# Performance work log

Measured on AMD Instinct MI355X. Metric: run time of the kernel, lower is better.

Reference implementation:

```python
import jax, jax.numpy as jnp
import numpy as np

N, IN_F, OUT_F, EMB = 8192, 256, 128, 16

def setup_inputs() -> dict:
    key = jax.random.key(0)
    ks = jax.random.split(key, 6)
    s_in, s_out = 1.0 / np.sqrt(IN_F), 1.0 / np.sqrt(OUT_F)
    return {
        "h": jax.random.normal(ks[0], (N, IN_F), jnp.float32),
        "eps": jax.random.normal(ks[1], (N, OUT_F), jnp.float32),
        "a_str": jax.random.uniform(ks[2], (N, N), jnp.float32),  # precomputed exp_adj kernel (positive)
        "W_fc": jax.random.normal(ks[3], (IN_F, OUT_F), jnp.float32) * s_in,
        "W_k": jax.random.normal(ks[4], (OUT_F, EMB), jnp.float32) * s_out,
        "W_q": jax.random.normal(ks[5], (OUT_F, EMB), jnp.float32) * s_out,
    }

def reference(h, eps, a_str, W_fc, W_k, W_q):
    # h0 = fc(h); h <- N(0,1) sample (eps) + h0
    hh = eps + h @ W_fc                      # [N, OUT_F]
    k = hh @ W_k                             # [N, EMB]
    q = hh @ W_q                             # [N, EMB]
    a_att = jax.nn.softmax(k @ q.T, axis=-1) # [N, N]
    a = a_str * a_att                        # elementwise structural mask
    a = a / jnp.sum(a, axis=-1, keepdims=True)  # renormalize rows
    return a @ hh                            # [N, OUT_F]
```

## Files before the change

### kernel.cpp

```cpp
#include <hip/hip_runtime.h>
#include <hip/hip_bf16.h>

#define NN   8192
#define INF_ 256
#define OF   128
#define EMBD 16
#define QB   32
#define JB   128
#define NST  (NN / JB)

typedef __attribute__((ext_vector_type(4))) float f32x4;
typedef __attribute__((ext_vector_type(8))) short s16x8;

__device__ __forceinline__ unsigned short f2bf(float x) {
  unsigned u = __builtin_bit_cast(unsigned, x);
  return (unsigned short)((u + 0x7FFFu + ((u >> 16) & 1u)) >> 16);
}

__device__ __forceinline__ float fexp2(float x) {
#if __has_builtin(__builtin_amdgcn_exp2f)
  return __builtin_amdgcn_exp2f(x);
#else
  return exp2f(x);
#endif
}

__global__ __launch_bounds__(256) void k_hh(const float* __restrict__ h,
                                            const float* __restrict__ eps,
                                            const float* __restrict__ Wfc,
                                            float* __restrict__ hh) {
  const int o  = threadIdx.x & (OF - 1);
  const int rh = threadIdx.x >> 7;
  const int i0 = blockIdx.x * 8 + rh * 4;
  float a0 = eps[(size_t)(i0 + 0) * OF + o];
  float a1 = eps[(size_t)(i0 + 1) * OF + o];
  float a2 = eps[(size_t)(i0 + 2) * OF + o];
  float a3 = eps[(size_t)(i0 + 3) * OF + o];
  const float* h0 = h + (size_t)(i0 + 0) * INF_;
  const float* h1 = h + (size_t)(i0 + 1) * INF_;
  const float* h2 = h + (size_t)(i0 + 2) * INF_;
  const float* h3 = h + (size_t)(i0 + 3) * INF_;
#pragma unroll 4
  for (int kk = 0; kk < INF_; ++kk) {
    const float wv = Wfc[(size_t)kk * OF + o];
    a0 = fmaf(h0[kk], wv, a0);
    a1 = fmaf(h1[kk], wv, a1);
    a2 = fmaf(h2[kk], wv, a2);
    a3 = fmaf(h3[kk], wv, a3);
  }
  hh[(size_t)(i0 + 0) * OF + o] = a0;
  hh[(size_t)(i0 + 1) * OF + o] = a1;
  hh[(size_t)(i0 + 2) * OF + o] = a2;
  hh[(size_t)(i0 + 3) * OF + o] = a3;
}

__global__ __launch_bounds__(256) void k_kq(const float* __restrict__ hh,
                                            const float* __restrict__ Wk,
                                            const float* __restrict__ Wq,
                                            float* __restrict__ kp,
                                            float* __restrict__ qp) {
  const int t = blockIdx.x * 256 + threadIdx.x;
  const int i = t >> 5;
  const int c = t & 31;
  const int e = c & 15;
  const float* W = (c < 16) ? Wk : Wq;
  const float* hr = hh + (size_t)i * OF;
  float s0 = 0.f, s1 = 0.f;
#pragma unroll 8
  for (int o = 0; o < OF; o += 2) {
    s0 = fmaf(hr[o], W[o * EMBD + e], s0);
    s1 = fmaf(hr[o + 1], W[(o + 1) * EMBD + e], s1);
  }
  const float s = s0 + s1;
  if (c < 16) kp[(size_t)i * EMBD + e] = s * 1.4426950408889634f;
  else        qp[(size_t)i * EMBD + e] = s;
}

__global__ __launch_bounds__(256) void k_tr(const float* __restrict__ hh,
                                            short* __restrict__ hhT) {
  __shared__ float tile[64][65];
  const int i0 = blockIdx.x * 64;
  const int o0 = blockIdx.y * 64;
  const int c = threadIdx.x & 63;
  const int r = threadIdx.x >> 6;
#pragma unroll
  for (int rr = 0; rr < 16; ++rr) {
    const int ii = rr * 4 + r;
    tile[ii][c] = hh[(size_t)(i0 + ii) * OF + o0 + c];
  }
  __syncthreads();
#pragma unroll
  for (int rr = 0; rr < 16; ++rr) {
    const int oo = rr * 4 + r;
    hhT[(size_t)(o0 + oo) * NN + i0 + c] = (short)f2bf(tile[c][oo]);
  }
}

__global__ __launch_bounds__(512, 1) void k_attn(const float* __restrict__ Astr,
                                                 const float* __restrict__ kp,
                                                 const float* __restrict__ qp,
                                                 const short* __restrict__ hhT,
                                                 float* __restrict__ out) {
  __shared__ __align__(16) float qbuf[2][JB * 20];
  __shared__ __align__(16) short wbuf[2][QB * JB];
  __shared__ float fscale[2][QB];
  __shared__ float dfin[QB];

  const int tid = threadIdx.x;
  const int l   = tid & 63;
  const int w   = tid >> 6;
  const int row = tid >> 4;
  const int g   = tid & 15;
  const int rt  = w >> 2;
  const int ctp = w & 3;
  const int h4  = l >> 4;
  const int ln  = l & 15;
  const int rb  = blockIdx.x * QB;
  const int jr  = tid >> 2;
  const int e4  = tid & 3;

  float kreg[16];
  {
    const f32x4* kv = (const f32x4*)(kp + (size_t)(rb + row) * EMBD);
#pragma unroll
    for (int i = 0; i < 4; ++i) {
      f32x4 v = kv[i];
      kreg[i * 4 + 0] = v.x; kreg[i * 4 + 1] = v.y;
      kreg[i * 4 + 2] = v.z; kreg[i * 4 + 3] = v.w;
    }
  }
  f32x4 acc0 = {0.f, 0.f, 0.f, 0.f};
  f32x4 acc1 = {0.f, 0.f, 0.f, 0.f};
  float mrun = -1e30f;
  float dpart = 0.f;

  const size_t arow = (size_t)(rb + row) * NN;
  const int swz_w = (row & 7) << 3;
  const int ra    = rt * 16 + ln;
  const int swz_r = (ra & 7) << 3;

  {
    f32x4 v = *(const f32x4*)(qp + (size_t)jr * EMBD + e4 * 4);
    *(f32x4*)&qbuf[0][jr * 20 + e4 * 4] = v;
  }
  float aA[8], aB[8];
#pragma unroll
  for (int jj = 0; jj < 8; ++jj) aA[jj] = Astr[arow + g + 16 * jj];
  __syncthreads();

  auto STEP = [&](int t, float (&acur)[8], float (&anxt)[8], int par) {
    const int jb = t * JB;
    const int tn = (t + 1 < NST) ? (t + 1) : 0;
    const int jn = tn * JB;
    f32x4 qv = *(const f32x4*)(qp + (size_t)(jn + jr) * EMBD + e4 * 4);
    s16x8 bfr[2][4];
#pragma unroll
    for (int cc = 0; cc < 2; ++cc) {
      const size_t bbase = (size_t)(ctp * 32 + cc * 16 + ln) * NN + jb + h4 * 8;
#pragma unroll
      for (int kt = 0; kt < 4; ++kt)
        bfr[cc][kt] = *(const s16x8*)(hhT + bbase + kt * 32);
    }
#pragma unroll
    for (int jj = 0; jj < 8; ++jj) anxt[jj] = Astr[arow + jn + g + 16 * jj];
    float s[8];
#pragma unroll
    for (int jj = 0; jj < 8; ++jj) {
      const float* qr = &qbuf[par][(g + 16 * jj) * 20];
      const f32x4 q0 = *(const f32x4*)(qr + 0);
      const f32x4 q1 = *(const f32x4*)(qr + 4);
      const f32x4 q2 = *(const f32x4*)(qr + 8);
      const f32x4 q3 = *(const f32x4*)(qr + 12);
      float t0 = kreg[0] * q0.x, t1 = kreg[1] * q0.y;
      t0 = fmaf(kreg[2],  q0.z, t0); t1 = fmaf(kreg[3],  q0.w, t1);
      t0 = fmaf(kreg[4],  q1.x, t0); t1 = fmaf(kreg[5],  q1.y, t1);
      t0 = fmaf(kreg[6],  q1.z, t0); t1 = fmaf(kreg[7],  q1.w, t1);
      t0 = fmaf(kreg[8],  q2.x, t0); t1 = fmaf(kreg[9],  q2.y, t1);
      t0 = fmaf(kreg[10], q2.z, t0); t1 = fmaf(kreg[11], q2.w, t1);
      t0 = fmaf(kreg[12], q3.x, t0); t1 = fmaf(kreg[13], q3.y, t1);
      t0 = fmaf(kreg[14], q3.z, t0); t1 = fmaf(kreg[15], q3.w, t1);
      s[jj] = t0 + t1;
    }
    float tmax = s[0];
#pragma unroll
    for (int jj = 1; jj < 8; ++jj) tmax = fmaxf(tmax, s[jj]);
    tmax = fmaxf(tmax, __shfl_xor(tmax, 1, 16));
    tmax = fmaxf(tmax, __shfl_xor(tmax, 2, 16));
    tmax = fmaxf(tmax, __shfl_xor(tmax, 4, 16));
    tmax = fmaxf(tmax, __shfl_xor(tmax, 8, 16));
    const float mnew = fmaxf(mrun, tmax);
    const float f = fexp2(mrun - mnew);
    mrun = mnew;
    dpart *= f;
#pragma unroll
    for (int jj = 0; jj < 8; ++jj) {
      const float wv = acur[jj] * fexp2(s[jj] - mnew);
      dpart += wv;
      wbuf[par][row * JB + ((g + 16 * jj) ^ swz_w)] = (short)f2bf(wv);
    }
    if (g == 0) fscale[par][row] = f;
    *(f32x4*)&qbuf[par ^ 1][jr * 20 + e4 * 4] = qv;
    __syncthreads();
#pragma unroll
    for (int r = 0; r < 4; ++r) {
      const float fr = fscale[par][rt * 16 + 4 * h4 + r];
      acc0[r] *= fr;
      acc1[r] *= fr;
    }
    s16x8 afr[4];
#pragma unroll
    for (int kt = 0; kt < 4; ++kt)
      afr[kt] = *(const s16x8*)&wbuf[par][ra * JB + ((kt * 32 + h4 * 8) ^ swz_r)];
#pragma unroll
    for (int kt = 0; kt < 4; ++kt) {
      acc0 = __builtin_amdgcn_mfma_f32_16x16x32_bf16(afr[kt], bfr[0][kt], acc0, 0, 0, 0);
      acc1 = __builtin_amdgcn_mfma_f32_16x16x32_bf16(afr[kt], bfr[1][kt], acc1, 0, 0, 0);
    }
  };

  for (int t = 0; t < NST; t += 2) {
    STEP(t,     aA, aB, 0);
    STEP(t + 1, aB, aA, 1);
  }

  float d = dpart;
  d += __shfl_xor(d, 1, 16);
  d += __shfl_xor(d, 2, 16);
  d += __shfl_xor(d, 4, 16);
  d += __shfl_xor(d, 8, 16);
  if (g == 0) dfin[row] = d;
  __syncthreads();
#pragma unroll
  for (int r = 0; r < 4; ++r) {
    const int lrow = rt * 16 + 4 * h4 + r;
    const float inv = 1.0f / dfin[lrow];
    float* orow = out + (size_t)(rb + lrow) * OF + ctp * 32 + ln;
    orow[0]  = acc0[r] * inv;
    orow[16] = acc1[r] * inv;
  }
}

extern "C" void kernel_launch(void* const* d_in, const int* in_sizes, int n_in,
                              void* d_out, int out_size, void* d_ws, size_t ws_size,
                              hipStream_t stream) {
  const float* h   = (const float*)d_in[0];
  const float* eps = (const float*)d_in[1];
  const float* As  = (const float*)d_in[2];
  const float* Wfc = (const float*)d_in[3];
  const float* Wk  = (const float*)d_in[4];
  const float* Wq  = (const float*)d_in[5];
  float* out = (float*)d_out;

  char* ws = (char*)d_ws;
  float* hh  = (float*)(ws);
  short* hhT = (short*)(ws + (4u << 20));
  float* kp  = (float*)(ws + (6u << 20));
  float* qp  = (float*)(ws + (6u << 20) + (512u << 10));

  k_hh<<<NN / 8, 256, 0, stream>>>(h, eps, Wfc, hh);
  k_kq<<<(NN * 32) / 256, 256, 0, stream>>>(hh, Wk, Wq, kp, qp);
  k_tr<<<dim3(NN / 64, OF / 64), 256, 0, stream>>>(hh, hhT);
  k_attn<<<NN / QB, 512, 0, stream>>>(As, kp, qp, hhT, out);
}
```

Before: 503.1 us.

## Split attention over key dimension with combine kernel, vectorize projections and loads

Splits the j-loop of the attention kernel four ways across a second grid dimension, writing partial accumulators and running max/denominator to workspace, then merges them in a new combine kernel using log-sum-exp rescaling. This gives 1024 blocks instead of 256 and raises launch_bounds occupancy to 4 blocks per CU. It also vectorizes the A_str loads into contiguous f32x4 reads with packed bf16 stores to a re-swizzled LDS buffer, and re-swizzles the q buffer. The hh and k/q projection kernels are rewritten to use f32x4 loads and FMAs. The cost is extra partial-result traffic of about 16 MB plus one more kernel launch.

```diff
diff --git a/kernel.cpp b/kernel.cpp
--- a/kernel.cpp
+++ b/kernel.cpp
@@ -1,13 +1,15 @@
 #include <hip/hip_runtime.h>
 #include <hip/hip_bf16.h>
 
-#define NN   8192
-#define INF_ 256
-#define OF   128
-#define EMBD 16
-#define QB   32
-#define JB   128
-#define NST  (NN / JB)
+#define NN     8192
+#define INF_   256
+#define OF     128
+#define EMBD   16
+#define QB     32
+#define JB     128
+#define NST    (NN / JB)
+#define JSPLIT 4
+#define NSTP   (NST / JSPLIT)
 
 typedef __attribute__((ext_vector_type(4))) float f32x4;
 typedef __attribute__((ext_vector_type(8))) short s16x8;
@@ -29,29 +31,27 @@
                                             const float* __restrict__ eps,
                                             const float* __restrict__ Wfc,
                                             float* __restrict__ hh) {
-  const int o  = threadIdx.x & (OF - 1);
-  const int rh = threadIdx.x >> 7;
-  const int i0 = blockIdx.x * 8 + rh * 4;
-  float a0 = eps[(size_t)(i0 + 0) * OF + o];
-  float a1 = eps[(size_t)(i0 + 1) * OF + o];
-  float a2 = eps[(size_t)(i0 + 2) * OF + o];
-  float a3 = eps[(size_t)(i0 + 3) * OF + o];
-  const float* h0 = h + (size_t)(i0 + 0) * INF_;
-  const float* h1 = h + (size_t)(i0 + 1) * INF_;
-  const float* h2 = h + (size_t)(i0 + 2) * INF_;
-  const float* h3 = h + (size_t)(i0 + 3) * INF_;
-#pragma unroll 4
-  for (int kk = 0; kk < INF_; ++kk) {
-    const float wv = Wfc[(size_t)kk * OF + o];
-    a0 = fmaf(h0[kk], wv, a0);
-    a1 = fmaf(h1[kk], wv, a1);
-    a2 = fmaf(h2[kk], wv, a2);
-    a3 = fmaf(h3[kk], wv, a3);
-  }
-  hh[(size_t)(i0 + 0) * OF + o] = a0;
-  hh[(size_t)(i0 + 1) * OF + o] = a1;
-  hh[(size_t)(i0 + 2) * OF + o] = a2;
-  hh[(size_t)(i0 + 3) * OF + o] = a3;
+  const int tx = threadIdx.x & 31;
+  const int ty = threadIdx.x >> 5;
+  const int i0 = blockIdx.x * 16 + ty * 2;
+  const int c  = tx * 4;
+  f32x4 a0 = *(const f32x4*)&eps[(size_t)i0 * OF + c];
+  f32x4 a1 = *(const f32x4*)&eps[(size_t)(i0 + 1) * OF + c];
+  const float* h0 = h + (size_t)i0 * INF_;
+  const float* h1 = h0 + INF_;
+#pragma unroll 2
+  for (int kk = 0; kk < INF_; kk += 4) {
+    const f32x4 ha = *(const f32x4*)&h0[kk];
+    const f32x4 hb = *(const f32x4*)&h1[kk];
+#pragma unroll
+    for (int u = 0; u < 4; ++u) {
+      const f32x4 wv = *(const f32x4*)&Wfc[(size_t)(kk + u) * OF + c];
+      a0 += ha[u] * wv;
+      a1 += hb[u] * wv;
+    }
+  }
+  *(f32x4*)&hh[(size_t)i0 * OF + c]       = a0;
+  *(f32x4*)&hh[(size_t)(i0 + 1) * OF + c] = a1;
 }
 
 __global__ __launch_bounds__(256) void k_kq(const float* __restrict__ hh,
@@ -59,21 +59,28 @@
                                             const float* __restrict__ Wq,
                                             float* __restrict__ kp,
                                             float* __restrict__ qp) {
-  const int t = blockIdx.x * 256 + threadIdx.x;
-  const int i = t >> 5;
-  const int c = t & 31;
-  const int e = c & 15;
-  const float* W = (c < 16) ? Wk : Wq;
+  const int t   = blockIdx.x * 256 + threadIdx.x;
+  const int i   = t >> 3;
+  const int sub = t & 7;
+  const float* W = (sub < 4) ? Wk : Wq;
+  const int e    = (sub & 3) * 4;
   const float* hr = hh + (size_t)i * OF;
-  float s0 = 0.f, s1 = 0.f;
-#pragma unroll 8
-  for (int o = 0; o < OF; o += 2) {
-    s0 = fmaf(hr[o], W[o * EMBD + e], s0);
-    s1 = fmaf(hr[o + 1], W[(o + 1) * EMBD + e], s1);
-  }
-  const float s = s0 + s1;
-  if (c < 16) kp[(size_t)i * EMBD + e] = s * 1.4426950408889634f;
-  else        qp[(size_t)i * EMBD + e] = s;
+  f32x4 acc = {0.f, 0.f, 0.f, 0.f};
+#pragma unroll 4
+  for (int o = 0; o < OF; o += 4) {
+    const f32x4 hv = *(const f32x4*)&hr[o];
+#pragma unroll
+    for (int u = 0; u < 4; ++u) {
+      const f32x4 wv = *(const f32x4*)&W[(size_t)(o + u) * EMBD + e];
+      acc += hv[u] * wv;
+    }
+  }
+  if (sub < 4) {
+    acc *= 1.4426950408889634f;
+    *(f32x4*)&kp[(size_t)i * EMBD + e] = acc;
+  } else {
+    *(f32x4*)&qp[(size_t)i * EMBD + e] = acc;
+  }
 }
 
 __global__ __launch_bounds__(256) void k_tr(const float* __restrict__ hh,
@@ -96,15 +103,15 @@
   }
 }
 
-__global__ __launch_bounds__(512, 1) void k_attn(const float* __restrict__ Astr,
+__global__ __launch_bounds__(512, 4) void k_attn(const float* __restrict__ Astr,
                                                  const float* __restrict__ kp,
                                                  const float* __restrict__ qp,
                                                  const short* __restrict__ hhT,
-                                                 float* __restrict__ out) {
-  __shared__ __align__(16) float qbuf[2][JB * 20];
+                                                 float* __restrict__ accP,
+                                                 float* __restrict__ mdP) {
+  __shared__ __align__(16) float qbuf[2][JB * EMBD];
   __shared__ __align__(16) short wbuf[2][QB * JB];
   __shared__ float fscale[2][QB];
-  __shared__ float dfin[QB];
 
   const int tid = threadIdx.x;
   const int l   = tid & 63;
@@ -116,6 +123,8 @@
   const int h4  = l >> 4;
   const int ln  = l & 15;
   const int rb  = blockIdx.x * QB;
+  const int p   = blockIdx.y;
+  const int t0  = p * NSTP;
   const int jr  = tid >> 2;
   const int e4  = tid & 3;
 
@@ -135,22 +144,23 @@
   float dpart = 0.f;
 
   const size_t arow = (size_t)(rb + row) * NN;
-  const int swz_w = (row & 7) << 3;
-  const int ra    = rt * 16 + ln;
-  const int swz_r = (ra & 7) << 3;
+  const int swzw = row & 7;
+  const int ra   = rt * 16 + ln;
+  const int qsw  = g & 7;
 
   {
-    f32x4 v = *(const f32x4*)(qp + (size_t)jr * EMBD + e4 * 4);
-    *(f32x4*)&qbuf[0][jr * 20 + e4 * 4] = v;
-  }
-  float aA[8], aB[8];
-#pragma unroll
-  for (int jj = 0; jj < 8; ++jj) aA[jj] = Astr[arow + g + 16 * jj];
+    f32x4 v = *(const f32x4*)(qp + (size_t)(t0 * JB + jr) * EMBD + e4 * 4);
+    const int gi = (jr * 4 + e4) ^ ((jr >> 3) & 7);
+    *(f32x4*)&qbuf[0][gi * 4] = v;
+  }
+  f32x4 aA[2], aB[2];
+  aA[0] = *(const f32x4*)(Astr + arow + t0 * JB + g * 8);
+  aA[1] = *(const f32x4*)(Astr + arow + t0 * JB + g * 8 + 4);
   __syncthreads();
 
-  auto STEP = [&](int t, float (&acur)[8], float (&anxt)[8], int par) {
+  auto STEP = [&](int t, f32x4 (&acur)[2], f32x4 (&anxt)[2], int par) {
     const int jb = t * JB;
-    const int tn = (t + 1 < NST) ? (t + 1) : 0;
+    const int tn = (t + 1 < t0 + NSTP) ? (t + 1) : t0;
     const int jn = tn * JB;
     f32x4 qv = *(const f32x4*)(qp + (size_t)(jn + jr) * EMBD + e4 * 4);
     s16x8 bfr[2][4];
@@ -161,25 +171,25 @@
       for (int kt = 0; kt < 4; ++kt)
         bfr[cc][kt] = *(const s16x8*)(hhT + bbase + kt * 32);
     }
-#pragma unroll
-    for (int jj = 0; jj < 8; ++jj) anxt[jj] = Astr[arow + jn + g + 16 * jj];
+    anxt[0] = *(const f32x4*)(Astr + arow + jn + g * 8);
+    anxt[1] = *(const f32x4*)(Astr + arow + jn + g * 8 + 4);
     float s[8];
 #pragma unroll
     for (int jj = 0; jj < 8; ++jj) {
-      const float* qr = &qbuf[par][(g + 16 * jj) * 20];
-      const f32x4 q0 = *(const f32x4*)(qr + 0);
-      const f32x4 q1 = *(const f32x4*)(qr + 4);
-      const f32x4 q2 = *(const f32x4*)(qr + 8);
-      const f32x4 q3 = *(const f32x4*)(qr + 12);
-      float t0 = kreg[0] * q0.x, t1 = kreg[1] * q0.y;
-      t0 = fmaf(kreg[2],  q0.z, t0); t1 = fmaf(kreg[3],  q0.w, t1);
-      t0 = fmaf(kreg[4],  q1.x, t0); t1 = fmaf(kreg[5],  q1.y, t1);
-      t0 = fmaf(kreg[6],  q1.z, t0); t1 = fmaf(kreg[7],  q1.w, t1);
-      t0 = fmaf(kreg[8],  q2.x, t0); t1 = fmaf(kreg[9],  q2.y, t1);
-      t0 = fmaf(kreg[10], q2.z, t0); t1 = fmaf(kreg[11], q2.w, t1);
-      t0 = fmaf(kreg[12], q3.x, t0); t1 = fmaf(kreg[13], q3.y, t1);
-      t0 = fmaf(kreg[14], q3.z, t0); t1 = fmaf(kreg[15], q3.w, t1);
-      s[jj] = t0 + t1;
+      const int r4 = (g * 8 + jj) * 4;
+      const f32x4 q0 = *(const f32x4*)&qbuf[par][((r4 + 0) ^ qsw) * 4];
+      const f32x4 q1 = *(const f32x4*)&qbuf[par][((r4 + 1) ^ qsw) * 4];
+      const f32x4 q2 = *(const f32x4*)&qbuf[par][((r4 + 2) ^ qsw) * 4];
+      const f32x4 q3 = *(const f32x4*)&qbuf[par][((r4 + 3) ^ qsw) * 4];
+      float u0 = kreg[0] * q0.x, u1 = kreg[1] * q0.y;
+      u0 = fmaf(kreg[2],  q0.z, u0); u1 = fmaf(kreg[3],  q0.w, u1);
+      u0 = fmaf(kreg[4],  q1.x, u0); u1 = fmaf(kreg[5],  q1.y, u1);
+      u0 = fmaf(kreg[6],  q1.z, u0); u1 = fmaf(kreg[7],  q1.w, u1);
+      u0 = fmaf(kreg[8],  q2.x, u0); u1 = fmaf(kreg[9],  q2.y, u1);
+      u0 = fmaf(kreg[10], q2.z, u0); u1 = fmaf(kreg[11], q2.w, u1);
+      u0 = fmaf(kreg[12], q3.x, u0); u1 = fmaf(kreg[13], q3.y, u1);
+      u0 = fmaf(kreg[14], q3.z, u0); u1 = fmaf(kreg[15], q3.w, u1);
+      s[jj] = u0 + u1;
     }
     float tmax = s[0];
 #pragma unroll
@@ -192,14 +202,22 @@
     const float f = fexp2(mrun - mnew);
     mrun = mnew;
     dpart *= f;
-#pragma unroll
-    for (int jj = 0; jj < 8; ++jj) {
-      const float wv = acur[jj] * fexp2(s[jj] - mnew);
-      dpart += wv;
-      wbuf[par][row * JB + ((g + 16 * jj) ^ swz_w)] = (short)f2bf(wv);
-    }
+    s16x8 wpack;
+    {
+      const float* ac = (const float*)&acur[0];
+#pragma unroll
+      for (int jj = 0; jj < 8; ++jj) {
+        const float wv = ac[jj] * fexp2(s[jj] - mnew);
+        dpart += wv;
+        wpack[jj] = (short)f2bf(wv);
+      }
+    }
+    *(s16x8*)&wbuf[par][row * JB + ((g ^ swzw) * 8)] = wpack;
     if (g == 0) fscale[par][row] = f;
-    *(f32x4*)&qbuf[par ^ 1][jr * 20 + e4 * 4] = qv;
+    {
+      const int gi = (jr * 4 + e4) ^ ((jr >> 3) & 7);
+      *(f32x4*)&qbuf[par ^ 1][gi * 4] = qv;
+    }
     __syncthreads();
 #pragma unroll
     for (int r = 0; r < 4; ++r) {
@@ -210,7 +228,7 @@
     s16x8 afr[4];
 #pragma unroll
     for (int kt = 0; kt < 4; ++kt)
-      afr[kt] = *(const s16x8*)&wbuf[par][ra * JB + ((kt * 32 + h4 * 8) ^ swz_r)];
+      afr[kt] = *(const s16x8*)&wbuf[par][ra * JB + (((kt * 4 + h4) ^ (ra & 7)) * 8)];
 #pragma unroll
     for (int kt = 0; kt < 4; ++kt) {
       acc0 = __builtin_amdgcn_mfma_f32_16x16x32_bf16(afr[kt], bfr[0][kt], acc0, 0, 0, 0);
@@ -218,7 +236,7 @@
     }
   };
 
-  for (int t = 0; t < NST; t += 2) {
+  for (int t = t0; t < t0 + NSTP; t += 2) {
     STEP(t,     aA, aB, 0);
     STEP(t + 1, aB, aA, 1);
   }
@@ -228,16 +246,42 @@
   d += __shfl_xor(d, 2, 16);
   d += __shfl_xor(d, 4, 16);
   d += __shfl_xor(d, 8, 16);
-  if (g == 0) dfin[row] = d;
-  __syncthreads();
+  if (g == 0) {
+    mdP[((size_t)p * NN + rb + row) * 2 + 0] = mrun;
+    mdP[((size_t)p * NN + rb + row) * 2 + 1] = d;
+  }
 #pragma unroll
   for (int r = 0; r < 4; ++r) {
     const int lrow = rt * 16 + 4 * h4 + r;
-    const float inv = 1.0f / dfin[lrow];
-    float* orow = out + (size_t)(rb + lrow) * OF + ctp * 32 + ln;
-    orow[0]  = acc0[r] * inv;
-    orow[16] = acc1[r] * inv;
-  }
+    float* orow = accP + ((size_t)p * NN + rb + lrow) * OF + ctp * 32 + ln;
+    orow[0]  = acc0[r];
+    orow[16] = acc1[r];
+  }
+}
+
+__global__ __launch_bounds__(256) void k_comb(const float* __restrict__ accP,
+                                              const float* __restrict__ mdP,
+                                              float* __restrict__ out) {
+  const int idx = blockIdx.x * 256 + threadIdx.x;
+  const int row = idx >> 7;
+  const int c   = idx & 127;
+  float m[JSPLIT], dd[JSPLIT];
+#pragma unroll
+  for (int pp = 0; pp < JSPLIT; ++pp) {
+    m[pp]  = mdP[((size_t)pp * NN + row) * 2 + 0];
+    dd[pp] = mdP[((size_t)pp * NN + row) * 2 + 1];
+  }
+  float M = m[0];
+#pragma unroll
+  for (int pp = 1; pp < JSPLIT; ++pp) M = fmaxf(M, m[pp]);
+  float D = 0.f, s = 0.f;
+#pragma unroll
+  for (int pp = 0; pp < JSPLIT; ++pp) {
+    const float f = fexp2(m[pp] - M);
+    D = fmaf(dd[pp], f, D);
+    s = fmaf(accP[((size_t)pp * NN + row) * OF + c], f, s);
+  }
+  out[(size_t)row * OF + c] = s / D;
 }
 
 extern "C" void kernel_launch(void* const* d_in, const int* in_sizes, int n_in,
@@ -252,13 +296,16 @@
   float* out = (float*)d_out;
 
   char* ws = (char*)d_ws;
-  float* hh  = (float*)(ws);
-  short* hhT = (short*)(ws + (4u << 20));
-  float* kp  = (float*)(ws + (6u << 20));
-  float* qp  = (float*)(ws + (6u << 20) + (512u << 10));
-
-  k_hh<<<NN / 8, 256, 0, stream>>>(h, eps, Wfc, hh);
-  k_kq<<<(NN * 32) / 256, 256, 0, stream>>>(hh, Wk, Wq, kp, qp);
+  float* hh   = (float*)(ws);
+  short* hhT  = (short*)(ws + (4u << 20));
+  float* kp   = (float*)(ws + (6u << 20));
+  float* qp   = (float*)(ws + (6u << 20) + (512u << 10));
+  float* accP = (float*)(ws + (7u << 20));
+  float* mdP  = (float*)(ws + (23u << 20));
+
+  k_hh<<<NN / 16, 256, 0, stream>>>(h, eps, Wfc, hh);
+  k_kq<<<(NN * 8) / 256, 256, 0, stream>>>(hh, Wk, Wq, kp, qp);
   k_tr<<<dim3(NN / 64, OF / 64), 256, 0, stream>>>(hh, hhT);
-  k_attn<<<NN / QB, 512, 0, stream>>>(As, kp, qp, hhT, out);
-}
+  k_attn<<<dim3(NN / QB, JSPLIT), 512, 0, stream>>>(As, kp, qp, hhT, accP, mdP);
+  k_comb<<<(NN * OF) / 256, 256, 0, stream>>>(accP, mdP, out);
+}
```

New measurement: 582.2 us. +15.7%, slower.
